# Kernel optimization log

Measured on AMD Instinct MI355X. Metric: run time of the kernel, lower is better.

## Reference

```python
import jax, jax.numpy as jnp
import numpy as np

B, S, HID = 2, 2048, 2048
NH, NKV, D = 16, 4, 128
EPS = 1e-6
THETA = 1000000.0
SCALE = D ** -0.5


def _rmsnorm(x, w):
    # per-head RMSNorm over last dim (head_dim)
    var = jnp.mean(x * x, axis=-1, keepdims=True)
    return x * jax.lax.rsqrt(var + EPS) * w


def _rope(pos, x):
    # neox-style rotary over full head_dim. x: [B,S,h,D], pos: [B,S]
    half = D // 2
    inv_freq = THETA ** (-jnp.arange(half, dtype=jnp.float32) / half)  # theta^(-2i/D)
    freqs = pos.astype(jnp.float32)[..., None] * inv_freq              # [B,S,half]
    cos = jnp.cos(freqs)[:, :, None, :]
    sin = jnp.sin(freqs)[:, :, None, :]
    x1, x2 = x[..., :half], x[..., half:]
    return jnp.concatenate([x1 * cos - x2 * sin, x2 * cos + x1 * sin], axis=-1)


def setup_inputs() -> dict:
    key = jax.random.key(0)
    ks = jax.random.split(key, 6)
    hidden_states = jax.random.normal(ks[0], (B, S, HID), dtype=jnp.float32)
    positions = jnp.tile(jnp.arange(S, dtype=jnp.int32)[None, :], (B, 1))
    sd = 0.02
    Wq = jax.random.normal(ks[1], (HID, NH * D), dtype=jnp.float32) * sd
    Wk = jax.random.normal(ks[2], (HID, NKV * D), dtype=jnp.float32) * sd
    Wv = jax.random.normal(ks[3], (HID, NKV * D), dtype=jnp.float32) * sd
    Wo = jax.random.normal(ks[4], (NH * D, HID), dtype=jnp.float32) * sd
    q_norm_w = jnp.ones((D,), dtype=jnp.float32)
    k_norm_w = jnp.ones((D,), dtype=jnp.float32)
    return {"hidden_states": hidden_states, "positions": positions,
            "Wq": Wq, "Wk": Wk, "Wv": Wv, "Wo": Wo,
            "q_norm_w": q_norm_w, "k_norm_w": k_norm_w}


def reference(hidden_states, positions, Wq, Wk, Wv, Wo, q_norm_w, k_norm_w):
    # QKV projections (no bias)
    q = (hidden_states @ Wq).reshape(B, S, NH, D)
    k = (hidden_states @ Wk).reshape(B, S, NKV, D)
    v = (hidden_states @ Wv).reshape(B, S, NKV, D)
    # per-head RMSNorm
    q = _rmsnorm(q, q_norm_w)
    k = _rmsnorm(k, k_norm_w)
    # rotary embedding
    q = _rope(positions, q)
    k = _rope(positions, k)
    # GQA: expand kv heads to q heads
    rep = NH // NKV
    k = jnp.repeat(k, rep, axis=2)  # [B,S,NH,D]
    v = jnp.repeat(v, rep, axis=2)
    # non-causal (ENCODER_ONLY) attention
    scores = jnp.einsum('bqhd,bkhd->bhqk', q, k) * SCALE
    attn = jax.nn.softmax(scores, axis=-1)
    ctx = jnp.einsum('bhqk,bkhd->bqhd', attn, v).reshape(B, S, NH * D)
    out = ctx @ Wo
    return out
```

## Files before the change

kernel.cpp:

```cpp
#include <hip/hip_runtime.h>

typedef unsigned short ushort_t;
typedef __attribute__((ext_vector_type(8))) short short8;
typedef __attribute__((ext_vector_type(4))) ushort_t ushort4_t;
typedef __attribute__((ext_vector_type(4))) float f32x4;

#define Bb 2
#define Ss 2048
#define HID 2048
#define NH 16
#define NKV 4
#define Dd 128
constexpr float EPS_ = 1e-6f;
constexpr float THETA_ = 1000000.0f;
constexpr float SCALE_ = 0.08838834764831845f;
constexpr float C2_ = 0.12753785f;
constexpr float THR_RAW_ = 23.5f;

__device__ __forceinline__ ushort_t f2bf(float x) {
  union { float f; unsigned u; } v; v.f = x;
  unsigned r = (v.u + 0x7fffu + ((v.u >> 16) & 1u)) >> 16;
  return (ushort_t)r;
}
__device__ __forceinline__ float bf2f(ushort_t u) {
  union { unsigned u; float f; } v; v.u = ((unsigned)u) << 16;
  return v.f;
}

typedef const __attribute__((address_space(1))) void* gas1_t;
typedef __attribute__((address_space(3))) void* las3_t;
__device__ __forceinline__ void gload_lds16(const void* g, void* l) {
  __builtin_amdgcn_global_load_lds((gas1_t)g, (las3_t)l, 16, 0, 0);
}

__device__ __forceinline__ void store_out(float* p, float v) { *p = v; }
__device__ __forceinline__ void store_out(ushort_t* p, float v) { *p = f2bf(v); }

__global__ __launch_bounds__(256) void prep_inputs(
    const float* __restrict__ hidden, ushort_t* __restrict__ Xbf,
    const float* __restrict__ Wq, const float* __restrict__ Wk,
    const float* __restrict__ Wv, const float* __restrict__ Wo,
    ushort_t* __restrict__ WqkvT, ushort_t* __restrict__ WoT) {
  __shared__ float tile[32][33];
  unsigned id = blockIdx.x;
  if (id < 4096u) {
    long i = ((long)id * 256 + threadIdx.x) * 8;
    float4 v0 = *(const float4*)(hidden + i);
    float4 v1 = *(const float4*)(hidden + i + 4);
    ushort4_t a, b;
    a[0] = f2bf(v0.x); a[1] = f2bf(v0.y); a[2] = f2bf(v0.z); a[3] = f2bf(v0.w);
    b[0] = f2bf(v1.x); b[1] = f2bf(v1.y); b[2] = f2bf(v1.z); b[3] = f2bf(v1.w);
    *(ushort4_t*)(Xbf + i) = a;
    *(ushort4_t*)(Xbf + i + 4) = b;
    return;
  }
  id -= 4096u;
  const float* src;
  ushort_t* dst;
  int C, tX;
  if (id < 4096u) {
    src = Wq; dst = WqkvT; C = 2048; tX = 64;
  } else if (id < 5120u) {
    id -= 4096u; src = Wk; dst = WqkvT + (long)2048 * 2048; C = 512; tX = 16;
  } else if (id < 6144u) {
    id -= 5120u; src = Wv; dst = WqkvT + (long)2560 * 2048; C = 512; tX = 16;
  } else {
    id -= 6144u; src = Wo; dst = WoT; C = 2048; tX = 64;
  }
  const int R = 2048;
  int c0 = (id % tX) * 32, r0 = (id / tX) * 32;
  int tx = threadIdx.x & 31, ty = threadIdx.x >> 5;
#pragma unroll
  for (int j = 0; j < 4; j++)
    tile[ty + j * 8][tx] = src[(long)(r0 + ty + j * 8) * C + c0 + tx];
  __syncthreads();
#pragma unroll
  for (int j = 0; j < 4; j++)
    dst[(long)(c0 + ty + j * 8) * R + r0 + tx] = f2bf(tile[tx][ty + j * 8]);
}

template <typename OutT>
__global__ __launch_bounds__(256) void gemm_bt(
    const ushort_t* __restrict__ A, const ushort_t* __restrict__ Bt,
    OutT* __restrict__ C, int M, int N, int K) {
  __shared__ __align__(16) ushort_t As[128 * 32];
  __shared__ __align__(16) ushort_t Bs[128 * 32];
  const int t = threadIdx.x;
  const int wave = t >> 6, lane = t & 63;
  const int wr = wave >> 1, wc = wave & 1;
  const int quad = lane >> 4, l16 = lane & 15;

  unsigned gx = gridDim.x;
  unsigned nwg = gx * gridDim.y;
  unsigned lin = blockIdx.y * gx + blockIdx.x;
  if ((nwg & 7u) == 0u) {
    unsigned cpx = nwg >> 3;
    lin = (lin & 7u) * cpx + (lin >> 3);
  }
  const long bm = (long)(lin / gx) * 128;
  const long bn = (long)(lin % gx) * 128;

  f32x4 acc[4][4] = {};

  const int srow = t >> 2, schunk = t & 3;
  const ushort_t* aSrc = A + (bm + srow) * (long)K + schunk * 8;
  const ushort_t* bSrc = Bt + (bn + srow) * (long)K + schunk * 8;
  const int ldsOff = srow * 32 + schunk * 8;

  for (int k0 = 0; k0 < K; k0 += 32) {
    __syncthreads();
    gload_lds16(aSrc + k0, &As[ldsOff]);
    gload_lds16(aSrc + (long)64 * K + k0, &As[ldsOff + 64 * 32]);
    gload_lds16(bSrc + k0, &Bs[ldsOff]);
    gload_lds16(bSrc + (long)64 * K + k0, &Bs[ldsOff + 64 * 32]);
    __syncthreads();
    short8 af[4], bf[4];
#pragma unroll
    for (int i = 0; i < 4; i++) {
      af[i] = *(const short8*)&As[(wr * 64 + i * 16 + l16) * 32 + quad * 8];
      bf[i] = *(const short8*)&Bs[(wc * 64 + i * 16 + l16) * 32 + quad * 8];
    }
#pragma unroll
    for (int i = 0; i < 4; i++)
#pragma unroll
      for (int j = 0; j < 4; j++)
        acc[i][j] = __builtin_amdgcn_mfma_f32_16x16x32_bf16(af[i], bf[j], acc[i][j], 0, 0, 0);
  }
#pragma unroll
  for (int i = 0; i < 4; i++)
#pragma unroll
    for (int j = 0; j < 4; j++)
#pragma unroll
      for (int r = 0; r < 4; r++) {
        long rr = bm + wr * 64 + i * 16 + quad * 4 + r;
        long cc = bn + wc * 64 + j * 16 + l16;
        store_out(&C[rr * N + cc], acc[i][j][r]);
      }
}

template <typename OutT>
__global__ __launch_bounds__(512) void gemm256_bt(
    const ushort_t* __restrict__ A, const ushort_t* __restrict__ Bt,
    OutT* __restrict__ C, int M, int N, int K) {
  __shared__ __align__(16) ushort_t As[2][256 * 64];
  __shared__ __align__(16) ushort_t Bs[2][256 * 64];
  const int t = threadIdx.x;
  const int wave = t >> 6, lane = t & 63;
  const int wm = wave >> 2, wn = wave & 3;
  const int quad = lane >> 4, l16 = lane & 15;

  unsigned gx = gridDim.x;
  unsigned nwg = gx * gridDim.y;
  unsigned lin = blockIdx.y * gx + blockIdx.x;
  if ((nwg & 7u) == 0u) {
    unsigned cpx = nwg >> 3;
    lin = (lin & 7u) * cpx + (lin >> 3);
  }
  const long bm = (long)(lin / gx) * 256;
  const long bn = (long)(lin % gx) * 256;

  auto stageA = [&](int kt, int ih, int bi) {
    const int k0 = kt * 64;
#pragma unroll
    for (int it = 0; it < 2; it++) {
      int ci = t + it * 512;
      int lr = ci >> 3, cl = ci & 7;
      int row = ((lr & 64) << 1) | (ih << 6) | (lr & 63);
      int cg = cl ^ (row & 7);
      gload_lds16(A + (bm + row) * (long)K + k0 + cg * 8, &As[bi][row * 64 + cl * 8]);
    }
  };
  auto stageB = [&](int kt, int jh, int bi) {
    const int k0 = kt * 64;
#pragma unroll
    for (int it = 0; it < 2; it++) {
      int ci = t + it * 512;
      int lr = ci >> 3, cl = ci & 7;
      int row = ((lr & 96) << 1) | (jh << 5) | (lr & 31);
      int cg = cl ^ (row & 7);
      gload_lds16(Bt + (bn + row) * (long)K + k0 + cg * 8, &Bs[bi][row * 64 + cl * 8]);
    }
  };

  f32x4 acc[8][4] = {};
  short8 af[2][4], bf0[2][2], bf1[2][2];

  const int nt = K >> 6;
  stageA(0, 0, 0); stageA(0, 1, 0); stageB(0, 0, 0); stageB(0, 1, 0);
  stageA(1, 0, 1); stageB(1, 0, 1);
  asm volatile("s_waitcnt vmcnt(4)" ::: "memory");
  __builtin_amdgcn_sched_barrier(0);
  __builtin_amdgcn_s_barrier();
  __builtin_amdgcn_sched_barrier(0);

  const int raBase = (wm * 128 + l16) * 64;
  const int rbBase = (wn * 64 + l16) * 64;
  const int sw = l16 & 7;

  for (int ti = 0; ti < nt; ti++) {
    const int cb = ti & 1;
    const ushort_t* as_ = As[cb];
    const ushort_t* bs_ = Bs[cb];

#pragma unroll
    for (int kk = 0; kk < 2; kk++) {
      int ch = ((kk * 4 + quad) ^ sw) * 8;
#pragma unroll
      for (int di = 0; di < 4; di++)
        af[kk][di] = *(const short8*)&as_[raBase + di * 1024 + ch];
#pragma unroll
      for (int dj = 0; dj < 2; dj++)
        bf0[kk][dj] = *(const short8*)&bs_[rbBase + dj * 1024 + ch];
    }
    if (ti + 1 < nt) stageA(ti + 1, 1, cb ^ 1);
    __builtin_amdgcn_sched_barrier(0);
    __builtin_amdgcn_s_barrier();
    __builtin_amdgcn_sched_barrier(0);
    __builtin_amdgcn_s_setprio(1);
#pragma unroll
    for (int di = 0; di < 4; di++)
#pragma unroll
      for (int dj = 0; dj < 2; dj++)
#pragma unroll
        for (int kk = 0; kk < 2; kk++)
          acc[di][dj] = __builtin_amdgcn_mfma_f32_16x16x32_bf16(af[kk][di], bf0[kk][dj], acc[di][dj], 0, 0, 0);
    __builtin_amdgcn_s_setprio(0);
    __builtin_amdgcn_sched_barrier(0);
    __builtin_amdgcn_s_barrier();
    __builtin_amdgcn_sched_barrier(0);

#pragma unroll
    for (int kk = 0; kk < 2; kk++) {
      int ch = ((kk * 4 + quad) ^ sw) * 8;
#pragma unroll
      for (int dj = 0; dj < 2; dj++)
        bf1[kk][dj] = *(const short8*)&bs_[rbBase + (2 + dj) * 1024 + ch];
    }
    if (ti + 1 < nt) stageB(ti + 1, 1, cb ^ 1);
    __builtin_amdgcn_sched_barrier(0);
    __builtin_amdgcn_s_barrier();
    __builtin_amdgcn_sched_barrier(0);
    __builtin_amdgcn_s_setprio(1);
#pragma unroll
    for (int di = 0; di < 4; di++)
#pragma unroll
      for (int dj = 0; dj < 2; dj++)
#pragma unroll
        for (int kk = 0; kk < 2; kk++)
          acc[di][2 + dj] = __builtin_amdgcn_mfma_f32_16x16x32_bf16(af[kk][di], bf1[kk][dj], acc[di][2 + dj], 0, 0, 0);
    __builtin_amdgcn_s_setprio(0);
    __builtin_amdgcn_sched_barrier(0);
    __builtin_amdgcn_s_barrier();
    __builtin_amdgcn_sched_barrier(0);

#pragma unroll
    for (int kk = 0; kk < 2; kk++) {
      int ch = ((kk * 4 + quad) ^ sw) * 8;
#pragma unroll
      for (int di = 0; di < 4; di++)
        af[kk][di] = *(const short8*)&as_[raBase + (4 + di) * 1024 + ch];
    }
    if (ti + 2 < nt) stageA(ti + 2, 0, cb);
    __builtin_amdgcn_sched_barrier(0);
    __builtin_amdgcn_s_barrier();
    __builtin_amdgcn_sched_barrier(0);
    __builtin_amdgcn_s_setprio(1);
#pragma unroll
    for (int di = 0; di < 4; di++)
#pragma unroll
      for (int dj = 0; dj < 2; dj++)
#pragma unroll
        for (int kk = 0; kk < 2; kk++)
          acc[4 + di][dj] = __builtin_amdgcn_mfma_f32_16x16x32_bf16(af[kk][di], bf0[kk][dj], acc[4 + di][dj], 0, 0, 0);
    __builtin_amdgcn_s_setprio(0);
    __builtin_amdgcn_sched_barrier(0);
    __builtin_amdgcn_s_barrier();
    __builtin_amdgcn_sched_barrier(0);

    if (ti + 2 < nt) stageB(ti + 2, 0, cb);
    __builtin_amdgcn_sched_barrier(0);
    __builtin_amdgcn_s_barrier();
    __builtin_amdgcn_sched_barrier(0);
    __builtin_amdgcn_s_setprio(1);
#pragma unroll
    for (int di = 0; di < 4; di++)
#pragma unroll
      for (int dj = 0; dj < 2; dj++)
#pragma unroll
        for (int kk = 0; kk < 2; kk++)
          acc[4 + di][2 + dj] = __builtin_amdgcn_mfma_f32_16x16x32_bf16(af[kk][di], bf1[kk][dj], acc[4 + di][2 + dj], 0, 0, 0);
    __builtin_amdgcn_s_setprio(0);
    if (ti + 2 < nt) {
      asm volatile("s_waitcnt vmcnt(4)" ::: "memory");
    } else if (ti + 1 < nt) {
      asm volatile("s_waitcnt vmcnt(0)" ::: "memory");
    }
    __builtin_amdgcn_sched_barrier(0);
    __builtin_amdgcn_s_barrier();
    __builtin_amdgcn_sched_barrier(0);
  }

#pragma unroll
  for (int i = 0; i < 8; i++)
#pragma unroll
    for (int j = 0; j < 4; j++)
#pragma unroll
      for (int r = 0; r < 4; r++) {
        long rr = bm + wm * 128 + i * 16 + quad * 4 + r;
        long cc = bn + wn * 64 + j * 16 + l16;
        store_out(&C[rr * N + cc], acc[i][j][r]);
      }
}

__global__ __launch_bounds__(256) void rmsnorm_rope_tv(
    ushort_t* __restrict__ qkv, const int* __restrict__ positions,
    const float* __restrict__ qw, const float* __restrict__ kw,
    ushort_t* __restrict__ Vt) {
  __shared__ ushort_t tile[64][65];
  unsigned bx = blockIdx.x;
  if (bx < 20480u) {
    int gw = bx * 4 + (threadIdx.x >> 6);
    int lane = threadIdx.x & 63;
    int bs = gw / 20, h = gw % 20;
    ushort_t* src = qkv + (long)bs * 3072 + h * 128;
    float x0 = bf2f(src[lane]), x1 = bf2f(src[lane + 64]);
    float ss = x0 * x0 + x1 * x1;
#pragma unroll
    for (int off = 32; off; off >>= 1) ss += __shfl_xor(ss, off);
    float r = rsqrtf(ss * (1.0f / 128.0f) + EPS_);
    const float* w = (h < 16) ? qw : kw;
    x0 = x0 * r * w[lane];
    x1 = x1 * r * w[lane + 64];
    float pos = (float)positions[bs];
    float inv_freq = powf(THETA_, -(float)lane * (1.0f / 64.0f));
    float f = pos * inv_freq;
    float sn, cs;
    sincosf(f, &sn, &cs);
    float o0 = x0 * cs - x1 * sn;
    float o1 = x1 * cs + x0 * sn;
    src[lane] = f2bf(o0);
    src[lane + 64] = f2bf(o1);
  } else {
    unsigned id = bx - 20480u;
    int bxo = id & 31, byo = (id >> 5) & 1, bh = id >> 6;
    int s0 = bxo * 64, d0 = byo * 64;
    int b = bh >> 2, hk = bh & 3;
    int tx = threadIdx.x & 63, ty = threadIdx.x >> 6;
#pragma unroll
    for (int j = 0; j < 16; j++) {
      int sl = j * 4 + ty;
      tile[sl][tx] = qkv[(long)(b * Ss + s0 + sl) * 3072 + 2560 + hk * 128 + d0 + tx];
    }
    __syncthreads();
    const long vtbase = (long)bh * Dd * Ss;
#pragma unroll
    for (int j = 0; j < 16; j++) {
      int dl = j * 4 + ty;
      Vt[vtbase + (long)(d0 + dl) * Ss + s0 + tx] = tile[tx][dl];
    }
  }
}

__global__ __launch_bounds__(512) void flash_attn(
    const ushort_t* __restrict__ qkv, const ushort_t* __restrict__ Vt,
    ushort_t* __restrict__ ctx) {
  __shared__ __align__(16) ushort_t Ks[2][64 * 128];
  __shared__ __align__(16) ushort_t Vs[2][128 * 64];
  __shared__ __align__(16) ushort_t Ps[8][16 * 64];
  const int qt = blockIdx.x, h = blockIdx.y, b = blockIdx.z;
  const int hk = h >> 2;
  const int t = threadIdx.x, wave = t >> 6, lane = t & 63;
  const int quad = lane >> 4, l16 = lane & 15;

  const ushort_t* qp = qkv + (long)(b * Ss + qt * 128) * 3072 + h * 128;
  const ushort_t* kp = qkv + (long)(b * Ss) * 3072 + 2048 + hk * 128;
  const ushort_t* vp = Vt + ((long)(b * NKV + hk) * Dd) * Ss;

  auto stage = [&](int kt, int bi) {
    const int k0 = kt * 64;
#pragma unroll
    for (int it = 0; it < 2; it++) {
      int tt = t + it * 512;
      int row = tt >> 4, cl = tt & 15, cg = cl ^ (row & 15);
      gload_lds16(kp + (long)(k0 + row) * 3072 + cg * 8, &Ks[bi][tt * 8]);
    }
#pragma unroll
    for (int it = 0; it < 2; it++) {
      int tt = t + it * 512;
      int row = tt >> 3, cl = tt & 7, cg = cl ^ (row & 7);
      gload_lds16(vp + (long)row * Ss + k0 + cg * 8, &Vs[bi][tt * 8]);
    }
  };

  stage(0, 0);

  short8 qf[4];
  {
    const ushort_t* qrow = qp + (long)(wave * 16 + l16) * 3072 + quad * 8;
#pragma unroll
    for (int kc = 0; kc < 4; kc++)
      qf[kc] = *(const short8*)(qrow + kc * 32);
  }

  float m_i = -1e30f;
  float l_acc = 0.f;
  f32x4 o[8] = {};

  asm volatile("s_waitcnt vmcnt(0)" ::: "memory");
  __syncthreads();

  int cur = 0;
  for (int kt = 0; kt < Ss / 64; kt++) {
    if (kt + 1 < Ss / 64) stage(kt + 1, cur ^ 1);

    f32x4 sa[4] = {};
    __builtin_amdgcn_s_setprio(1);
#pragma unroll
    for (int kc = 0; kc < 4; kc++) {
#pragma unroll
      for (int nt = 0; nt < 4; nt++) {
        int brow = nt * 16 + l16;
        short8 kfr = *(const short8*)&Ks[cur][brow * 128 + (((kc * 4 + quad) ^ (brow & 15)) * 8)];
        sa[nt] = __builtin_amdgcn_mfma_f32_16x16x32_bf16(kfr, qf[kc], sa[nt], 0, 0, 0);
      }
    }
    __builtin_amdgcn_s_setprio(0);

    float pmax = sa[0][0];
#pragma unroll
    for (int nt = 0; nt < 4; nt++)
#pragma unroll
      for (int r = 0; r < 4; r++) pmax = fmaxf(pmax, sa[nt][r]);

    bool upd = __any(pmax > m_i + THR_RAW_);
    float alpha = 1.0f;
    if (upd) {
      float mx = fmaxf(pmax, __shfl_xor(pmax, 16));
      mx = fmaxf(mx, __shfl_xor(mx, 32));
      float mnew = fmaxf(m_i, mx);
      alpha = __builtin_amdgcn_exp2f((m_i - mnew) * C2_);
      m_i = mnew;
      l_acc *= alpha;
    }

    float mC2 = m_i * C2_;
    float rs = 0.f;
#pragma unroll
    for (int nt = 0; nt < 4; nt++) {
      int cbase = l16 * 64 + ((nt * 2 + (quad >> 1)) ^ (l16 & 7)) * 8 + (quad & 1) * 4;
#pragma unroll
      for (int r = 0; r < 4; r++) {
        float p = __builtin_amdgcn_exp2f(__builtin_fmaf(sa[nt][r], C2_, -mC2));
        rs += p;
        union { float f; unsigned u; } pv; pv.f = p;
        Ps[wave][cbase + r] = (ushort_t)((pv.u + 0x8000u) >> 16);
      }
    }
    l_acc += rs;

    if (upd) {
      float ar0 = __shfl(alpha, quad * 4 + 0);
      float ar1 = __shfl(alpha, quad * 4 + 1);
      float ar2 = __shfl(alpha, quad * 4 + 2);
      float ar3 = __shfl(alpha, quad * 4 + 3);
#pragma unroll
      for (int dt = 0; dt < 8; dt++) {
        o[dt][0] *= ar0; o[dt][1] *= ar1; o[dt][2] *= ar2; o[dt][3] *= ar3;
      }
    }
    asm volatile("s_waitcnt lgkmcnt(0)" ::: "memory");

    __builtin_amdgcn_s_setprio(1);
#pragma unroll
    for (int kc = 0; kc < 2; kc++) {
      int arow = l16;
      short8 af = *(const short8*)&Ps[wave][arow * 64 + (((kc * 4 + quad) ^ (arow & 7)) * 8)];
#pragma unroll
      for (int dt = 0; dt < 8; dt++) {
        int brow = dt * 16 + l16;
        short8 bfr = *(const short8*)&Vs[cur][brow * 64 + (((kc * 4 + quad) ^ (brow & 7)) * 8)];
        o[dt] = __builtin_amdgcn_mfma_f32_16x16x32_bf16(af, bfr, o[dt], 0, 0, 0);
      }
    }
    __builtin_amdgcn_s_setprio(0);

    asm volatile("s_waitcnt vmcnt(0)" ::: "memory");
    __syncthreads();
    cur ^= 1;
  }

  float lt = l_acc + __shfl_xor(l_acc, 16);
  lt += __shfl_xor(lt, 32);
  float linv = 1.0f / lt;
  float lr0 = __shfl(linv, quad * 4 + 0);
  float lr1 = __shfl(linv, quad * 4 + 1);
  float lr2 = __shfl(linv, quad * 4 + 2);
  float lr3 = __shfl(linv, quad * 4 + 3);
  const long obase = (long)(b * Ss + qt * 128 + wave * 16) * (NH * Dd) + h * Dd;
#pragma unroll
  for (int dt = 0; dt < 8; dt++) {
    int col = dt * 16 + l16;
    ctx[obase + (long)(quad * 4 + 0) * (NH * Dd) + col] = f2bf(o[dt][0] * lr0);
    ctx[obase + (long)(quad * 4 + 1) * (NH * Dd) + col] = f2bf(o[dt][1] * lr1);
    ctx[obase + (long)(quad * 4 + 2) * (NH * Dd) + col] = f2bf(o[dt][2] * lr2);
    ctx[obase + (long)(quad * 4 + 3) * (NH * Dd) + col] = f2bf(o[dt][3] * lr3);
  }
}

extern "C" void kernel_launch(void* const* d_in, const int* in_sizes, int n_in,
                              void* d_out, int out_size, void* d_ws, size_t ws_size,
                              hipStream_t stream) {
  const float* hidden = (const float*)d_in[0];
  const int* positions = (const int*)d_in[1];
  const float* Wq = (const float*)d_in[2];
  const float* Wk = (const float*)d_in[3];
  const float* Wv = (const float*)d_in[4];
  const float* Wo = (const float*)d_in[5];
  const float* qw = (const float*)d_in[6];
  const float* kw = (const float*)d_in[7];
  float* out = (float*)d_out;

  char* ws = (char*)d_ws;
  ushort_t* Xbf = (ushort_t*)(ws);
  ushort_t* WqkvT = (ushort_t*)(ws + (16l << 20));
  ushort_t* WoT = (ushort_t*)(ws + (28l << 20));
  ushort_t* qkvb = (ushort_t*)(ws + (36l << 20));
  ushort_t* Vt = (ushort_t*)(ws + (60l << 20));
  ushort_t* ctx = Xbf;

  prep_inputs<<<14336, 256, 0, stream>>>(hidden, Xbf, Wq, Wk, Wv, Wo, WqkvT, WoT);

  gemm256_bt<ushort_t><<<dim3(3072 / 256, 4096 / 256), 512, 0, stream>>>(Xbf, WqkvT, qkvb, 4096, 3072, 2048);

  rmsnorm_rope_tv<<<20480 + 512, 256, 0, stream>>>(qkvb, positions, qw, kw, Vt);

  flash_attn<<<dim3(Ss / 128, NH, Bb), 512, 0, stream>>>(qkvb, Vt, ctx);

  gemm_bt<float><<<dim3(2048 / 128, 4096 / 128), 256, 0, stream>>>(ctx, WoT, out, 4096, 2048, 2048);
}
```

Measured before the change: 335.8 us.

## Fuse RMSNorm, RoPE and V transpose into the QKV GEMM epilogue

The QKV GEMM epilogue now applies per-head RMSNorm and rotary embedding to Q/K tiles in registers and writes V transposed via an LDS staging buffer. This removes the separate rmsnorm_rope_tv launch and its full read-modify-write of the QKV buffer. Cross-wave reductions and rotate-half partners go through LDS, which adds epilogue synchronisation. The shared arena is larger, which may affect occupancy.

New measurement: 364.8 us. +8.6%, slower.

```diff
diff --git a/kernel.cpp b/kernel.cpp
--- a/kernel.cpp
+++ b/kernel.cpp
@@ -16,6 +16,7 @@
 constexpr float SCALE_ = 0.08838834764831845f;
 constexpr float C2_ = 0.12753785f;
 constexpr float THR_RAW_ = 23.5f;
+constexpr float NLOG2TH64_ = -0.311430759430f;
 
 __device__ __forceinline__ ushort_t f2bf(float x) {
   union { float f; unsigned u; } v; v.f = x;
@@ -138,12 +139,15 @@
       }
 }
 
-template <typename OutT>
-__global__ __launch_bounds__(512) void gemm256_bt(
+__global__ __launch_bounds__(512) void gemm256_qkv(
     const ushort_t* __restrict__ A, const ushort_t* __restrict__ Bt,
-    OutT* __restrict__ C, int M, int N, int K) {
-  __shared__ __align__(16) ushort_t As[2][256 * 64];
-  __shared__ __align__(16) ushort_t Bs[2][256 * 64];
+    ushort_t* __restrict__ qkvb, ushort_t* __restrict__ Vt,
+    const int* __restrict__ positions,
+    const float* __restrict__ qw, const float* __restrict__ kw) {
+  __shared__ __align__(16) char arena[133632];
+  ushort_t* Asb = (ushort_t*)arena;
+  ushort_t* Bsb = (ushort_t*)(arena + 65536);
+  const int K = 2048;
   const int t = threadIdx.x;
   const int wave = t >> 6, lane = t & 63;
   const int wm = wave >> 2, wn = wave & 3;
@@ -167,7 +171,7 @@
       int lr = ci >> 3, cl = ci & 7;
       int row = ((lr & 64) << 1) | (ih << 6) | (lr & 63);
       int cg = cl ^ (row & 7);
-      gload_lds16(A + (bm + row) * (long)K + k0 + cg * 8, &As[bi][row * 64 + cl * 8]);
+      gload_lds16(A + (bm + row) * (long)K + k0 + cg * 8, &Asb[bi * 16384 + row * 64 + cl * 8]);
     }
   };
   auto stageB = [&](int kt, int jh, int bi) {
@@ -178,7 +182,7 @@
       int lr = ci >> 3, cl = ci & 7;
       int row = ((lr & 96) << 1) | (jh << 5) | (lr & 31);
       int cg = cl ^ (row & 7);
-      gload_lds16(Bt + (bn + row) * (long)K + k0 + cg * 8, &Bs[bi][row * 64 + cl * 8]);
+      gload_lds16(Bt + (bn + row) * (long)K + k0 + cg * 8, &Bsb[bi * 16384 + row * 64 + cl * 8]);
     }
   };
 
@@ -199,8 +203,8 @@
 
   for (int ti = 0; ti < nt; ti++) {
     const int cb = ti & 1;
-    const ushort_t* as_ = As[cb];
-    const ushort_t* bs_ = Bs[cb];
+    const ushort_t* as_ = Asb + cb * 16384;
+    const ushort_t* bs_ = Bsb + cb * 16384;
 
 #pragma unroll
     for (int kk = 0; kk < 2; kk++) {
@@ -300,65 +304,115 @@
     __builtin_amdgcn_sched_barrier(0);
   }
 
+  const long b = bm >> 11;
+  const int colBase = (int)bn + wn * 64;
+
+  if (bn >= 2560) {
+    const int VP = 260;
+    ushort_t* vt = (ushort_t*)arena;
+#pragma unroll
+    for (int i = 0; i < 8; i++)
+#pragma unroll
+      for (int j = 0; j < 4; j++) {
+        int vd = wn * 64 + j * 16 + l16;
+        int vs = wm * 128 + i * 16 + quad * 4;
+        ushort4_t pk;
+        pk[0] = f2bf(acc[i][j][0]); pk[1] = f2bf(acc[i][j][1]);
+        pk[2] = f2bf(acc[i][j][2]); pk[3] = f2bf(acc[i][j][3]);
+        *(ushort4_t*)&vt[vd * VP + vs] = pk;
+      }
+    __syncthreads();
+    const int vOff = (int)bn - 2560;
+    const long vbase = (b * 512 + vOff) * 2048 + (bm & 2047);
+#pragma unroll
+    for (int it = 0; it < 32; it++) {
+      int c = it * 512 + t;
+      int vd = c >> 6;
+      int vs4 = (c & 63) << 2;
+      ushort4_t v = *(const ushort4_t*)&vt[vd * VP + vs4];
+      *(ushort4_t*)&Vt[vbase + (long)vd * 2048 + vs4] = v;
+    }
+    return;
+  }
+
+  float* ssb = (float*)arena;
+  ushort_t* et = (ushort_t*)(arena + 4096);
+
+  float rv[8][4];
 #pragma unroll
   for (int i = 0; i < 8; i++)
 #pragma unroll
+    for (int r = 0; r < 4; r++) {
+      float s = acc[i][0][r] * acc[i][0][r];
+      s += acc[i][1][r] * acc[i][1][r];
+      s += acc[i][2][r] * acc[i][2][r];
+      s += acc[i][3][r] * acc[i][3][r];
+      s += __shfl_xor(s, 1); s += __shfl_xor(s, 2);
+      s += __shfl_xor(s, 4); s += __shfl_xor(s, 8);
+      rv[i][r] = s;
+    }
+  if (l16 == 0) {
+#pragma unroll
+    for (int i = 0; i < 8; i++)
+#pragma unroll
+      for (int r = 0; r < 4; r++)
+        ssb[wave * 128 + i * 16 + quad * 4 + r] = rv[i][r];
+  }
+  __syncthreads();
+#pragma unroll
+  for (int i = 0; i < 8; i++)
+#pragma unroll
+    for (int r = 0; r < 4; r++) {
+      float ss = rv[i][r] + ssb[(wave ^ 1) * 128 + i * 16 + quad * 4 + r];
+      rv[i][r] = rsqrtf(ss * (1.0f / 128.0f) + EPS_);
+    }
+  const float* wt = (colBase >= 2048) ? kw : qw;
+  float wv[4];
+#pragma unroll
+  for (int j = 0; j < 4; j++) wv[j] = wt[(wn & 1) * 64 + j * 16 + l16];
+
+  if (wave & 1) {
+#pragma unroll
+    for (int i = 0; i < 8; i++)
+#pragma unroll
+      for (int j = 0; j < 4; j++)
+#pragma unroll
+        for (int r = 0; r < 4; r++)
+          et[(wave >> 1) * 8192 + (i * 16 + quad * 4 + r) * 64 + j * 16 + l16] =
+              f2bf(acc[i][j][r] * rv[i][r] * wv[j]);
+    __syncthreads();
+    return;
+  }
+#pragma unroll
+  for (int i = 0; i < 8; i++)
+#pragma unroll
     for (int j = 0; j < 4; j++)
 #pragma unroll
-      for (int r = 0; r < 4; r++) {
-        long rr = bm + wm * 128 + i * 16 + quad * 4 + r;
-        long cc = bn + wn * 64 + j * 16 + l16;
-        store_out(&C[rr * N + cc], acc[i][j][r]);
-      }
-}
-
-__global__ __launch_bounds__(256) void rmsnorm_rope_tv(
-    ushort_t* __restrict__ qkv, const int* __restrict__ positions,
-    const float* __restrict__ qw, const float* __restrict__ kw,
-    ushort_t* __restrict__ Vt) {
-  __shared__ ushort_t tile[64][65];
-  unsigned bx = blockIdx.x;
-  if (bx < 20480u) {
-    int gw = bx * 4 + (threadIdx.x >> 6);
-    int lane = threadIdx.x & 63;
-    int bs = gw / 20, h = gw % 20;
-    ushort_t* src = qkv + (long)bs * 3072 + h * 128;
-    float x0 = bf2f(src[lane]), x1 = bf2f(src[lane + 64]);
-    float ss = x0 * x0 + x1 * x1;
-#pragma unroll
-    for (int off = 32; off; off >>= 1) ss += __shfl_xor(ss, off);
-    float r = rsqrtf(ss * (1.0f / 128.0f) + EPS_);
-    const float* w = (h < 16) ? qw : kw;
-    x0 = x0 * r * w[lane];
-    x1 = x1 * r * w[lane + 64];
-    float pos = (float)positions[bs];
-    float inv_freq = powf(THETA_, -(float)lane * (1.0f / 64.0f));
-    float f = pos * inv_freq;
-    float sn, cs;
-    sincosf(f, &sn, &cs);
-    float o0 = x0 * cs - x1 * sn;
-    float o1 = x1 * cs + x0 * sn;
-    src[lane] = f2bf(o0);
-    src[lane + 64] = f2bf(o1);
-  } else {
-    unsigned id = bx - 20480u;
-    int bxo = id & 31, byo = (id >> 5) & 1, bh = id >> 6;
-    int s0 = bxo * 64, d0 = byo * 64;
-    int b = bh >> 2, hk = bh & 3;
-    int tx = threadIdx.x & 63, ty = threadIdx.x >> 6;
-#pragma unroll
-    for (int j = 0; j < 16; j++) {
-      int sl = j * 4 + ty;
-      tile[sl][tx] = qkv[(long)(b * Ss + s0 + sl) * 3072 + 2560 + hk * 128 + d0 + tx];
-    }
-    __syncthreads();
-    const long vtbase = (long)bh * Dd * Ss;
-#pragma unroll
-    for (int j = 0; j < 16; j++) {
-      int dl = j * 4 + ty;
-      Vt[vtbase + (long)(d0 + dl) * Ss + s0 + tx] = tile[tx][dl];
-    }
-  }
+      for (int r = 0; r < 4; r++)
+        acc[i][j][r] = acc[i][j][r] * rv[i][r] * wv[j];
+  __syncthreads();
+
+  float invf[4];
+#pragma unroll
+  for (int j = 0; j < 4; j++)
+    invf[j] = exp2f((float)(j * 16 + l16) * NLOG2TH64_);
+#pragma unroll
+  for (int i = 0; i < 8; i++)
+#pragma unroll
+    for (int r = 0; r < 4; r++) {
+      long srow = bm + wm * 128 + i * 16 + quad * 4 + r;
+      float pos = (float)positions[srow];
+#pragma unroll
+      for (int j = 0; j < 4; j++) {
+        float x0 = acc[i][j][r];
+        float x1 = bf2f(et[(wave >> 1) * 8192 + (i * 16 + quad * 4 + r) * 64 + j * 16 + l16]);
+        float f = pos * invf[j];
+        float sn, cs;
+        sincosf(f, &sn, &cs);
+        qkvb[srow * 3072 + colBase + j * 16 + l16] = f2bf(x0 * cs - x1 * sn);
+        qkvb[srow * 3072 + colBase + 64 + j * 16 + l16] = f2bf(x1 * cs + x0 * sn);
+      }
+    }
 }
 
 __global__ __launch_bounds__(512) void flash_attn(
@@ -530,9 +584,8 @@
 
   prep_inputs<<<14336, 256, 0, stream>>>(hidden, Xbf, Wq, Wk, Wv, Wo, WqkvT, WoT);
 
-  gemm256_bt<ushort_t><<<dim3(3072 / 256, 4096 / 256), 512, 0, stream>>>(Xbf, WqkvT, qkvb, 4096, 3072, 2048);
-
-  rmsnorm_rope_tv<<<20480 + 512, 256, 0, stream>>>(qkvb, positions, qw, kw, Vt);
+  gemm256_qkv<<<dim3(3072 / 256, 4096 / 256), 512, 0, stream>>>(
+      Xbf, WqkvT, qkvb, Vt, positions, qw, kw);
 
   flash_attn<<<dim3(Ss / 128, NH, Bb), 512, 0, stream>>>(qkvb, Vt, ctx);
 
```
